# Kernel optimization log

Hardware: AMD Instinct MI355X
Metric: run time of the kernel (lower is better)

## Reference

```python
import jax, jax.numpy as jnp
import numpy as np

B, S = 8, 2048
CLIP, H, BN, NC = 512, 512, 256, 10
LN_EPS = 1e-5


def _ln(x, g, b):
    mu = x.mean(-1, keepdims=True)
    var = ((x - mu) ** 2).mean(-1, keepdims=True)
    return (x - mu) * jax.lax.rsqrt(var + LN_EPS) * g + b


def setup_inputs() -> dict:
    key = jax.random.key(0)
    ks = jax.random.split(key, 16)
    sc = lambda i, shp: jax.random.normal(ks[i], shp, jnp.float32) * 0.02
    inp = {
        "local_feat": jax.random.normal(ks[0], (B, S, CLIP), jnp.float32),
        "coords": jax.random.uniform(ks[1], (B, S, 3), jnp.float32),
        "mask": jax.random.randint(ks[2], (B, S), 0, 2) > 0,
        # node encoder
        "w_enc": sc(3, (CLIP, H)), "b_enc": jnp.zeros((H,), jnp.float32),
        "ln1_g": jnp.ones((H,), jnp.float32), "ln1_b": jnp.zeros((H,), jnp.float32),
        # attention projections
        "wq": sc(4, (H, H)), "bq": jnp.zeros((H,), jnp.float32),
        "wk": sc(5, (H, H)), "bk": jnp.zeros((H,), jnp.float32),
        "wv": sc(6, (H, H)), "bv": jnp.zeros((H,), jnp.float32),
        # bottleneck
        "w_bn": sc(7, (H, BN)), "b_bn": jnp.zeros((BN,), jnp.float32),
        "ln2_g": jnp.ones((BN,), jnp.float32), "ln2_b": jnp.zeros((BN,), jnp.float32),
        # classifier
        "w_c1": sc(8, (BN, BN // 2)), "b_c1": jnp.zeros((BN // 2,), jnp.float32),
        "w_c2": sc(9, (BN // 2, NC)), "b_c2": jnp.zeros((NC,), jnp.float32),
    }
    return inp


def reference(local_feat, coords, mask, w_enc, b_enc, ln1_g, ln1_b,
              wq, bq, wk, bk, wv, bv, w_bn, b_bn, ln2_g, ln2_b,
              w_c1, b_c1, w_c2, b_c2):
    # node encoder (dropout is identity in eval)
    h = jax.nn.relu(_ln(local_feat @ w_enc + b_enc, ln1_g, ln1_b))  # [B,S,H]

    # pairwise euclidean distance on (x,y), exp-modulated adjacency
    pos = coords[:, :, :2]
    diff = pos[:, :, None, :] - pos[:, None, :, :]              # [B,S,S,2]
    sq = jnp.sum(diff * diff, axis=-1)                          # [B,S,S]
    dist = jnp.sqrt(jnp.where(sq > 0, sq, 1.0))
    dist = jnp.where(sq > 0, dist, 0.0)
    spatial_adj = jnp.exp(-dist * 5.0)

    q = h @ wq + bq
    k = h @ wk + bk
    v = h @ wv + bv
    scores = jnp.einsum("bsd,btd->bst", q, k) / jnp.sqrt(jnp.float32(H))
    attn = jax.nn.softmax(scores, axis=-1) * spatial_adj        # [B,S,S]
    attn = jnp.where(mask[:, None, :], 0.0, attn)               # zero padded keys

    h_graph = jnp.einsum("bst,btd->bsd", attn, v)               # [B,S,H]
    out = jax.nn.relu(_ln(h_graph @ w_bn + b_bn, ln2_g, ln2_b)) # [B,S,BN]

    valid = (~mask)[:, :, None].astype(out.dtype)               # [B,S,1]
    pooled = (out * valid).sum(1) / jnp.clip(valid.sum(1), 1e-9, None)

    logits = jax.nn.relu(pooled @ w_c1 + b_c1) @ w_c2 + b_c2    # [B,NC]
    return logits, pooled
```

## Files before the change

kernel.cpp:

```cpp
#include <hip/hip_runtime.h>
#include <hip/hip_bf16.h>
#include <stdint.h>


typedef __hip_bfloat16 bf16_t;
typedef unsigned char u8;
typedef __attribute__((ext_vector_type(8))) short bf16x8;
typedef __attribute__((ext_vector_type(4))) float f32x4;

__device__ __forceinline__ void cp16_to_lds(const void* g, void* lds) {
  __builtin_amdgcn_global_load_lds(
      (__attribute__((address_space(1))) void*)(g),
      (__attribute__((address_space(3))) void*)(lds), 16, 0, 0);
}

__device__ __forceinline__ uint pk2(float a, float b) {
  bf16_t x = __float2bfloat16(a), y = __float2bfloat16(b);
  return ((uint)(*(ushort*)&y) << 16) | (*(ushort*)&x);
}
__device__ __forceinline__ float bflo(uint u) { return __uint_as_float(u << 16); }
__device__ __forceinline__ float bfhi(uint u) { return __uint_as_float(u & 0xffff0000u); }

__global__ __launch_bounds__(256) void gemm_bt(
    const bf16_t* __restrict__ A, const bf16_t* __restrict__ B,
    void* __restrict__ Cv, const float* __restrict__ bias, int biasStride,
    float scale, int K, long sA, long sB, long sC, int ldC, int mode)
{
  __shared__ __align__(16) char smem[32768];
  bf16_t* lA = (bf16_t*)smem;
  bf16_t* lB = (bf16_t*)(smem + 16384);
  const int z = blockIdx.z;
  A += (long)z * sA;
  B += (long)z * sB;
  const float* bz = bias ? bias + (long)z * biasStride : nullptr;
  const int m0 = blockIdx.y * 128, n0 = blockIdx.x * 128;
  const int tid = threadIdx.x;
  const int w = tid >> 6, lane = tid & 63;
  const int wm = w >> 1, wn = w & 1;

  const int rr = tid >> 2;
  const int cc = (((tid & 3) ^ ((tid >> 3) & 3)) * 8);
  const bf16_t* a0 = A + (long)(m0 + rr) * K + cc;
  const bf16_t* b0 = B + (long)(n0 + rr) * K + cc;
  const long rowskip = (long)64 * K;

  char* lAc = (char*)lA;
  char* lBc = (char*)lB;
  const int ofs0 = w * 1024;
  const int ofs1 = 4096 + w * 1024;

  f32x4 acc[4][4] = {};
  const int nkt = K >> 6;
  const int quad = lane >> 4;
  const int rsel = lane & 15;
  const int swz = (rsel >> 1) & 3;
  const int kchunkA = (quad ^ swz) * 8;

  for (int kt = 0; kt < nkt; ++kt) {
    __syncthreads();
    cp16_to_lds(a0,                 lAc + ofs0);
    cp16_to_lds(a0 + rowskip,       lAc + ofs1);
    cp16_to_lds(a0 + 32,            lAc + 8192 + ofs0);
    cp16_to_lds(a0 + 32 + rowskip,  lAc + 8192 + ofs1);
    cp16_to_lds(b0,                 lBc + ofs0);
    cp16_to_lds(b0 + rowskip,       lBc + ofs1);
    cp16_to_lds(b0 + 32,            lBc + 8192 + ofs0);
    cp16_to_lds(b0 + 32 + rowskip,  lBc + 8192 + ofs1);
    a0 += 64; b0 += 64;
    __syncthreads();

#pragma unroll
    for (int p = 0; p < 2; ++p) {
      const int pb = p * 4096;
      bf16x8 af[4], bfr[4];
#pragma unroll
      for (int i = 0; i < 4; ++i) {
        af[i]  = *(const bf16x8*)&lA[pb + (wm * 64 + i * 16 + rsel) * 32 + kchunkA];
        bfr[i] = *(const bf16x8*)&lB[pb + (wn * 64 + i * 16 + rsel) * 32 + kchunkA];
      }
#pragma unroll
      for (int i = 0; i < 4; ++i)
#pragma unroll
        for (int j = 0; j < 4; ++j)
          acc[i][j] = __builtin_amdgcn_mfma_f32_16x16x32_bf16(af[i], bfr[j], acc[i][j], 0, 0, 0);
    }
  }

  const int col = lane & 15;
  float bv4[4];
#pragma unroll
  for (int j = 0; j < 4; ++j) {
    const int ng = n0 + wn * 64 + j * 16 + col;
    bv4[j] = bz ? bz[ng] : 0.0f;
  }

  if (mode == 0) {
    char* stb = smem + w * 2176;
    const int nc0 = n0 + wn * 64;
#pragma unroll
    for (int i = 0; i < 4; ++i) {
      __syncthreads();
      bf16_t* st = (bf16_t*)stb;
#pragma unroll
      for (int j = 0; j < 4; ++j)
#pragma unroll
        for (int r = 0; r < 4; ++r)
          st[(quad * 4 + r) * 68 + j * 16 + col] =
              __float2bfloat16(acc[i][j][r] * scale + bv4[j]);
      __syncthreads();
      const int row16 = lane >> 2, cseg = lane & 3;
      const long mrow = m0 + wm * 64 + i * 16 + row16;
      bf16_t* cp = (bf16_t*)Cv + (long)z * sC + mrow * ldC + nc0 + cseg * 16;
      const char* sp = stb + row16 * 136 + cseg * 32;
#pragma unroll
      for (int hh = 0; hh < 2; ++hh) {
        uint2 aa = *(const uint2*)(sp + hh * 16);
        uint2 bb = *(const uint2*)(sp + hh * 16 + 8);
        uint4 vv; vv.x = aa.x; vv.y = aa.y; vv.z = bb.x; vv.w = bb.y;
        *(uint4*)(cp + hh * 8) = vv;
      }
    }
  } else {
#pragma unroll
    for (int j = 0; j < 4; ++j) {
      const int ng = n0 + wn * 64 + j * 16 + col;
#pragma unroll
      for (int i = 0; i < 4; ++i) {
        const int mg = m0 + wm * 64 + i * 16 + quad * 4;
#pragma unroll
        for (int r = 0; r < 4; ++r)
          ((float*)Cv)[(long)z * sC + (long)(mg + r) * ldC + ng] =
              acc[i][j][r] * scale + bv4[j];
      }
    }
  }
}

__global__ __launch_bounds__(256) void gemm_qkv(
    const bf16_t* __restrict__ A, const bf16_t* __restrict__ wT,
    const float* __restrict__ bias_cat, u8* __restrict__ o8,
    bf16_t* __restrict__ vT)
{
  __shared__ __align__(16) char smem[32768];
  bf16_t* lA = (bf16_t*)smem;
  bf16_t* lB = (bf16_t*)(smem + 16384);
  const int z = blockIdx.z;
  const bf16_t* B = wT + (long)(z + 1) * 262144;
  const float* bz = bias_cat + (long)z * 512;
  const int K = 512;
  const int m0 = blockIdx.y * 128, n0 = blockIdx.x * 128;
  const int tid = threadIdx.x;
  const int w = tid >> 6, lane = tid & 63;
  const int wm = w >> 1, wn = w & 1;

  const int rr = tid >> 2;
  const int cc = (((tid & 3) ^ ((tid >> 3) & 3)) * 8);
  const bf16_t* a0 = A + (long)(m0 + rr) * K + cc;
  const bf16_t* b0 = B + (long)(n0 + rr) * K + cc;
  const long rowskip = (long)64 * K;

  char* lAc = (char*)lA;
  char* lBc = (char*)lB;
  const int ofs0 = w * 1024;
  const int ofs1 = 4096 + w * 1024;

  f32x4 acc[4][4] = {};
  const int quad = lane >> 4;
  const int rsel = lane & 15;
  const int swz = (rsel >> 1) & 3;
  const int kchunkA = (quad ^ swz) * 8;

  for (int kt = 0; kt < 8; ++kt) {
    __syncthreads();
    cp16_to_lds(a0,                 lAc + ofs0);
    cp16_to_lds(a0 + rowskip,       lAc + ofs1);
    cp16_to_lds(a0 + 32,            lAc + 8192 + ofs0);
    cp16_to_lds(a0 + 32 + rowskip,  lAc + 8192 + ofs1);
    cp16_to_lds(b0,                 lBc + ofs0);
    cp16_to_lds(b0 + rowskip,       lBc + ofs1);
    cp16_to_lds(b0 + 32,            lBc + 8192 + ofs0);
    cp16_to_lds(b0 + 32 + rowskip,  lBc + 8192 + ofs1);
    a0 += 64; b0 += 64;
    __syncthreads();

#pragma unroll
    for (int p = 0; p < 2; ++p) {
      const int pb = p * 4096;
      bf16x8 af[4], bfr[4];
#pragma unroll
      for (int i = 0; i < 4; ++i) {
        af[i]  = *(const bf16x8*)&lA[pb + (wm * 64 + i * 16 + rsel) * 32 + kchunkA];
        bfr[i] = *(const bf16x8*)&lB[pb + (wn * 64 + i * 16 + rsel) * 32 + kchunkA];
      }
#pragma unroll
      for (int i = 0; i < 4; ++i)
#pragma unroll
        for (int j = 0; j < 4; ++j)
          acc[i][j] = __builtin_amdgcn_mfma_f32_16x16x32_bf16(af[i], bfr[j], acc[i][j], 0, 0, 0);
    }
  }

  const int col = lane & 15;
  float bv4[4];
#pragma unroll
  for (int j = 0; j < 4; ++j) bv4[j] = bz[n0 + wn * 64 + j * 16 + col];
  const int nc0 = n0 + wn * 64;

  if (z < 2) {
    u8* stb = (u8*)(smem + w * 2176);
    u8* O = o8 + (long)z * 8388608;
#pragma unroll
    for (int i = 0; i < 4; ++i) {
      __syncthreads();
#pragma unroll
      for (int j = 0; j < 4; ++j) {
        uint pk = 0;
        pk = __builtin_amdgcn_cvt_pk_fp8_f32(acc[i][j][0] + bv4[j],
                                             acc[i][j][1] + bv4[j], pk, false);
        pk = __builtin_amdgcn_cvt_pk_fp8_f32(acc[i][j][2] + bv4[j],
                                             acc[i][j][3] + bv4[j], pk, true);
        stb[(quad * 4 + 0) * 72 + j * 16 + col] = (u8)(pk);
        stb[(quad * 4 + 1) * 72 + j * 16 + col] = (u8)(pk >> 8);
        stb[(quad * 4 + 2) * 72 + j * 16 + col] = (u8)(pk >> 16);
        stb[(quad * 4 + 3) * 72 + j * 16 + col] = (u8)(pk >> 24);
      }
      __syncthreads();
      const int trow = lane >> 2, seg = lane & 3;
      const long mrow = m0 + wm * 64 + i * 16 + trow;
      *(uint4*)(O + mrow * 512 + nc0 + seg * 16) =
          *(const uint4*)(stb + trow * 72 + seg * 16);
    }
  } else {
    bf16_t* st = (bf16_t*)(smem + w * 2176);
    const int bt = blockIdx.y >> 4;
    const int t0g = (m0 & 2047) + wm * 64;
#pragma unroll
    for (int j = 0; j < 4; ++j) {
      __syncthreads();
#pragma unroll
      for (int i = 0; i < 4; ++i) {
        uint2 v2;
        v2.x = pk2(acc[i][j][0] + bv4[j], acc[i][j][1] + bv4[j]);
        v2.y = pk2(acc[i][j][2] + bv4[j], acc[i][j][3] + bv4[j]);
        *(uint2*)&st[col * 68 + i * 16 + quad * 4] = v2;
      }
      __syncthreads();
      const int drow = lane >> 2, seg = lane & 3;
      const int d = nc0 + j * 16 + drow;
      bf16_t* dst = vT + ((long)(bt * 512 + d)) * 2048 + t0g;
#pragma unroll
      for (int rd = 0; rd < 2; ++rd)
        *(uint4*)(dst + rd * 32 + seg * 8) =
            *(const uint4*)((const char*)st + drow * 136 + rd * 64 + seg * 16);
    }
  }
}

__global__ __launch_bounds__(256) void gemm_sc_fp8(
    const u8* __restrict__ A, const u8* __restrict__ B,
    bf16_t* __restrict__ C, float scale)
{
  __shared__ __align__(16) char smem[32768];
  const int K = 512;
  const int z = blockIdx.z;
  A += (long)z * 1048576;
  B += (long)z * 1048576;
  const int m0 = blockIdx.y * 128, n0 = blockIdx.x * 128;
  const int tid = threadIdx.x;
  const int w = tid >> 6, lane = tid & 63;
  const int wm = w >> 1, wn = w & 1;

  const int rr = tid >> 2;
  const int ccB = (((tid & 3) ^ ((tid >> 3) & 3)) * 16);
  const u8* a0 = A + (long)(m0 + rr) * K + ccB;
  const u8* b0 = B + (long)(n0 + rr) * K + ccB;
  const long rowskip = (long)64 * K;

  char* lAc = smem;
  char* lBc = smem + 16384;
  const int ofs0 = w * 1024;
  const int ofs1 = 4096 + w * 1024;

  f32x4 acc[4][4] = {};
  const int quad = lane >> 4;
  const int rsel = lane & 15;
  const int swz = (rsel >> 1) & 3;

  for (int kt = 0; kt < 4; ++kt) {
    __syncthreads();
    cp16_to_lds(a0,                  lAc + ofs0);
    cp16_to_lds(a0 + rowskip,        lAc + ofs1);
    cp16_to_lds(a0 + 64,             lAc + 8192 + ofs0);
    cp16_to_lds(a0 + 64 + rowskip,   lAc + 8192 + ofs1);
    cp16_to_lds(b0,                  lBc + ofs0);
    cp16_to_lds(b0 + rowskip,        lBc + ofs1);
    cp16_to_lds(b0 + 64,             lBc + 8192 + ofs0);
    cp16_to_lds(b0 + 64 + rowskip,   lBc + 8192 + ofs1);
    a0 += 128; b0 += 128;
    __syncthreads();

#pragma unroll
    for (int p = 0; p < 2; ++p) {
      const int pb = p * 8192;
#pragma unroll
      for (int ks = 0; ks < 2; ++ks) {
        const int gr = ((ks * 2 + (quad >> 1)) ^ swz) * 16 + (quad & 1) * 8;
        long av[4], bv[4];
#pragma unroll
        for (int i = 0; i < 4; ++i) {
          av[i] = *(const long*)(lAc + pb + (wm * 64 + i * 16 + rsel) * 64 + gr);
          bv[i] = *(const long*)(lBc + pb + (wn * 64 + i * 16 + rsel) * 64 + gr);
        }
#pragma unroll
        for (int i = 0; i < 4; ++i)
#pragma unroll
          for (int j = 0; j < 4; ++j)
            acc[i][j] = __builtin_amdgcn_mfma_f32_16x16x32_fp8_fp8(av[i], bv[j], acc[i][j], 0, 0, 0);
      }
    }
  }

  const int col = lane & 15;
  char* stb = smem + w * 2176;
  const int nc0 = n0 + wn * 64;
#pragma unroll
  for (int i = 0; i < 4; ++i) {
    __syncthreads();
    bf16_t* st = (bf16_t*)stb;
#pragma unroll
    for (int j = 0; j < 4; ++j)
#pragma unroll
      for (int r = 0; r < 4; ++r)
        st[(quad * 4 + r) * 68 + j * 16 + col] =
            __float2bfloat16(acc[i][j][r] * scale);
    __syncthreads();
    const int row16 = lane >> 2, cseg = lane & 3;
    const long mrow = m0 + wm * 64 + i * 16 + row16;
    bf16_t* cp = C + (long)z * 4194304 + mrow * 2048 + nc0 + cseg * 16;
    const char* sp = stb + row16 * 136 + cseg * 32;
#pragma unroll
    for (int hh = 0; hh < 2; ++hh) {
      uint2 aa = *(const uint2*)(sp + hh * 16);
      uint2 bb = *(const uint2*)(sp + hh * 16 + 8);
      uint4 vv; vv.x = aa.x; vv.y = aa.y; vv.z = bb.x; vv.w = bb.y;
      *(uint4*)(cp + hh * 8) = vv;
    }
  }
}

__global__ __launch_bounds__(256) void weight_prep(
    const float* __restrict__ w0, const float* __restrict__ w1,
    const float* __restrict__ w2, const float* __restrict__ w3,
    const float* __restrict__ w4,
    const float* __restrict__ bq, const float* __restrict__ bk,
    const float* __restrict__ bv,
    bf16_t* __restrict__ outT, float* __restrict__ bias_cat)
{
  const int z = blockIdx.z;
  const int N = (z == 4) ? 256 : 512;
  if (z == 4 && blockIdx.y >= 4) return;
  const float* in = (z == 0) ? w0 : (z == 1) ? w1 : (z == 2) ? w2 : (z == 3) ? w3 : w4;
  bf16_t* out = outT + (long)z * 262144;
  const int k0 = blockIdx.x * 64, n0 = blockIdx.y * 64;
  __shared__ bf16_t tile[64 * 66];
  const int tid = threadIdx.x;
  const int r = tid >> 2, c4 = tid & 3;
  const float* src = in + (long)(k0 + r) * N + n0 + c4 * 16;
  uint* dst = (uint*)&tile[r * 66 + c4 * 16];
  float4 f0 = ((const float4*)src)[0], f1 = ((const float4*)src)[1];
  float4 f2 = ((const float4*)src)[2], f3 = ((const float4*)src)[3];
  dst[0] = pk2(f0.x, f0.y); dst[1] = pk2(f0.z, f0.w);
  dst[2] = pk2(f1.x, f1.y); dst[3] = pk2(f1.z, f1.w);
  dst[4] = pk2(f2.x, f2.y); dst[5] = pk2(f2.z, f2.w);
  dst[6] = pk2(f3.x, f3.y); dst[7] = pk2(f3.z, f3.w);
  __syncthreads();
  bf16_t* og = out + (long)(n0 + r) * 512 + k0 + c4 * 16;
  uint ov[8];
#pragma unroll
  for (int j = 0; j < 16; j += 2) {
    const ushort lo = *(const ushort*)&tile[(c4 * 16 + j) * 66 + r];
    const ushort hi = *(const ushort*)&tile[(c4 * 16 + j + 1) * 66 + r];
    ov[j >> 1] = ((uint)hi << 16) | lo;
  }
  uint4 o0, o1;
  o0.x = ov[0]; o0.y = ov[1]; o0.z = ov[2]; o0.w = ov[3];
  o1.x = ov[4]; o1.y = ov[5]; o1.z = ov[6]; o1.w = ov[7];
  ((uint4*)og)[0] = o0;
  ((uint4*)og)[1] = o1;
  if (z >= 1 && z <= 3 && blockIdx.x == 0 && blockIdx.y == 0) {
    const float* bs = (z == 1) ? bq : (z == 2) ? bk : bv;
    bias_cat[(z - 1) * 512 + tid] = bs[tid];
    bias_cat[(z - 1) * 512 + 256 + tid] = bs[256 + tid];
  }
}

__global__ __launch_bounds__(256) void cast_bf16_v(
    const float4* __restrict__ in, uint2* __restrict__ o, int n4) {
  const int i = blockIdx.x * 256 + threadIdx.x;
  if (i < n4) {
    const float4 f = in[i];
    uint2 r; r.x = pk2(f.x, f.y); r.y = pk2(f.z, f.w);
    o[i] = r;
  }
}

__global__ __launch_bounds__(256) void ln_relu_h(
    bf16_t* __restrict__ X, const float* __restrict__ g, const float* __restrict__ b)
{
  const int tid = threadIdx.x;
  const int lane = tid & 63, w = tid >> 6;
  const long row = (long)blockIdx.x * 4 + w;
  bf16_t* xp = X + row * 512 + lane * 8;
  const uint4 pkv = *(const uint4*)xp;
  const uint va[4] = {pkv.x, pkv.y, pkv.z, pkv.w};
  float v[8];
  float s = 0.0f, q = 0.0f;
#pragma unroll
  for (int i = 0; i < 4; ++i) {
    v[2 * i] = bflo(va[i]); v[2 * i + 1] = bfhi(va[i]);
    s += v[2 * i] + v[2 * i + 1];
    q += v[2 * i] * v[2 * i] + v[2 * i + 1] * v[2 * i + 1];
  }
  for (int o = 32; o; o >>= 1) { s += __shfl_down(s, o); q += __shfl_down(q, o); }
  s = __shfl(s, 0); q = __shfl(q, 0);
  const float mu = s * (1.0f / 512.0f);
  const float rs = rsqrtf(q * (1.0f / 512.0f) - mu * mu + 1e-5f);
  const float4 g0 = ((const float4*)(g + lane * 8))[0], g1 = ((const float4*)(g + lane * 8))[1];
  const float4 b0 = ((const float4*)(b + lane * 8))[0], b1 = ((const float4*)(b + lane * 8))[1];
  const float gg[8] = {g0.x, g0.y, g0.z, g0.w, g1.x, g1.y, g1.z, g1.w};
  const float bb[8] = {b0.x, b0.y, b0.z, b0.w, b1.x, b1.y, b1.z, b1.w};
  uint ov[4];
#pragma unroll
  for (int i = 0; i < 4; ++i) {
    const float y0 = fmaxf((v[2 * i] - mu) * rs * gg[2 * i] + bb[2 * i], 0.0f);
    const float y1 = fmaxf((v[2 * i + 1] - mu) * rs * gg[2 * i + 1] + bb[2 * i + 1], 0.0f);
    ov[i] = pk2(y0, y1);
  }
  uint4 st; st.x = ov[0]; st.y = ov[1]; st.z = ov[2]; st.w = ov[3];
  *(uint4*)xp = st;
}

__global__ __launch_bounds__(256) void softmax_adj(
    bf16_t* __restrict__ SC, const float* __restrict__ coords,
    const int* __restrict__ mask)
{
  const int bs = blockIdx.x;
  const int b = bs >> 11, s = bs & 2047;
  const long base = (long)bs * 2048;
  const int tid = threadIdx.x;
  const uint4 pkv = *(const uint4*)(SC + base + tid * 8);
  const uint va[4] = {pkv.x, pkv.y, pkv.z, pkv.w};
  float rv[8];
  float mx = -3.0e38f;
#pragma unroll
  for (int i = 0; i < 4; ++i) {
    rv[2 * i] = bflo(va[i]); rv[2 * i + 1] = bfhi(va[i]);
    mx = fmaxf(mx, fmaxf(rv[2 * i], rv[2 * i + 1]));
  }
  for (int o = 32; o; o >>= 1) mx = fmaxf(mx, __shfl_down(mx, o));
  __shared__ float sm[8];
  const int w = tid >> 6, lane = tid & 63;
  if (!lane) sm[w] = mx;
  __syncthreads();
  mx = fmaxf(fmaxf(sm[0], sm[1]), fmaxf(sm[2], sm[3]));
  float sum = 0.0f;
#pragma unroll
  for (int i = 0; i < 8; ++i) { rv[i] = __expf(rv[i] - mx); sum += rv[i]; }
  for (int o = 32; o; o >>= 1) sum += __shfl_down(sum, o);
  if (!lane) sm[4 + w] = sum;
  __syncthreads();
  const float inv = 1.0f / (sm[4] + sm[5] + sm[6] + sm[7]);
  const float px = coords[((long)b * 2048 + s) * 3];
  const float py = coords[((long)b * 2048 + s) * 3 + 1];
  const int t0 = tid * 8;
  const float* cb = coords + ((long)b * 2048 + t0) * 3;
  const int* mb = mask + b * 2048 + t0;
  uint ov[4];
#pragma unroll
  for (int i = 0; i < 8; ++i) {
    const float dx = px - cb[i * 3], dy = py - cb[i * 3 + 1];
    const float adj = __expf(-5.0f * sqrtf(dx * dx + dy * dy));
    const float val = mb[i] ? 0.0f : rv[i] * inv * adj;
    bf16_t bt = __float2bfloat16(val);
    const ushort u = *(const ushort*)&bt;
    if (i & 1) ov[i >> 1] |= ((uint)u << 16);
    else       ov[i >> 1] = u;
  }
  uint4 st; st.x = ov[0]; st.y = ov[1]; st.z = ov[2]; st.w = ov[3];
  *(uint4*)(SC + base + t0) = st;
}

__global__ __launch_bounds__(256) void ln2_pool(
    const float* __restrict__ X, const float* __restrict__ g, const float* __restrict__ bt,
    const int* __restrict__ mask, float* __restrict__ pacc)
{
  const int tid = threadIdx.x;
  const int row0 = blockIdx.x * 16;
  const int w = tid >> 6, lane = tid & 63;
  __shared__ float sm[8];
  const float gv = g[tid], bv = bt[tid];
  float acc = 0.0f;
  for (int r = 0; r < 16; ++r) {
    const int row = row0 + r;
    const float x = X[(long)row * 256 + tid];
    float s = x, q = x * x;
    for (int o = 32; o; o >>= 1) { s += __shfl_down(s, o); q += __shfl_down(q, o); }
    if (!lane) { sm[w] = s; sm[4 + w] = q; }
    __syncthreads();
    const float S = sm[0] + sm[1] + sm[2] + sm[3];
    const float Q = sm[4] + sm[5] + sm[6] + sm[7];
    const float mu = S * (1.0f / 256.0f);
    const float rs = rsqrtf(Q * (1.0f / 256.0f) - mu * mu + 1e-5f);
    const float y = fmaxf((x - mu) * rs * gv + bv, 0.0f);
    if (!mask[row]) acc += y;
    __syncthreads();
  }
  atomicAdd(&pacc[(row0 >> 11) * 256 + tid], acc);
}

__global__ __launch_bounds__(256) void classifier_k(
    const float* __restrict__ pacc, const int* __restrict__ mask,
    const float* __restrict__ w1, const float* __restrict__ b1,
    const float* __restrict__ w2, const float* __restrict__ b2,
    float* __restrict__ out)
{
  const int tid = threadIdx.x;
  __shared__ float pooled[2048];
  __shared__ float hidden[1024];
  __shared__ float cnt[8];
  if (tid < 8) cnt[tid] = 0.0f;
  __syncthreads();
  {
    const int* mb = mask + tid * 64;
    int c = 0;
#pragma unroll 8
    for (int i = 0; i < 64; ++i) c += mb[i] ? 0 : 1;
    atomicAdd(&cnt[tid >> 5], (float)c);
  }
  __syncthreads();
  for (int i = tid; i < 2048; i += 256) {
    const float p = pacc[i] / fmaxf(cnt[i >> 8], 1e-9f);
    pooled[i] = p;
    out[80 + i] = p;
  }
  __syncthreads();
  for (int o = tid; o < 1024; o += 256) {
    const int bb = o >> 7, j = o & 127;
    float s = b1[j];
    const float* pb = pooled + bb * 256;
    for (int c = 0; c < 256; ++c) s += pb[c] * w1[c * 128 + j];
    hidden[o] = fmaxf(s, 0.0f);
  }
  __syncthreads();
  if (tid < 80) {
    const int bb = tid / 10, j = tid - bb * 10;
    float s = b2[j];
    const float* hb = hidden + bb * 128;
    for (int c = 0; c < 128; ++c) s += hb[c] * w2[c * 10 + j];
    out[tid] = s;
  }
}

extern "C" void kernel_launch(void* const* d_in, const int* in_sizes, int n_in,
                              void* d_out, int out_size, void* d_ws, size_t ws_size,
                              hipStream_t stream)
{
  const float* lf   = (const float*)d_in[0];
  const float* co   = (const float*)d_in[1];
  const int*   mk   = (const int*)d_in[2];
  const float* wenc = (const float*)d_in[3];
  const float* benc = (const float*)d_in[4];
  const float* g1   = (const float*)d_in[5];
  const float* be1  = (const float*)d_in[6];
  const float* wq   = (const float*)d_in[7];
  const float* bq   = (const float*)d_in[8];
  const float* wk   = (const float*)d_in[9];
  const float* bk   = (const float*)d_in[10];
  const float* wv   = (const float*)d_in[11];
  const float* bvp  = (const float*)d_in[12];
  const float* wbn  = (const float*)d_in[13];
  const float* bbn  = (const float*)d_in[14];
  const float* g2   = (const float*)d_in[15];
  const float* be2  = (const float*)d_in[16];
  const float* w1   = (const float*)d_in[17];
  const float* b1   = (const float*)d_in[18];
  const float* w2   = (const float*)d_in[19];
  const float* b2   = (const float*)d_in[20];
  float* out = (float*)d_out;
  char* ws = (char*)d_ws;

  bf16_t* featb = (bf16_t*)(ws + 0);
  bf16_t* wT    = (bf16_t*)(ws + 16777216);
  bf16_t* wencT = wT;
  bf16_t* wbnT  = wT + 4 * 262144;
  float*  bias_cat = (float*)(ws + 19398656);
  bf16_t* h     = (bf16_t*)(ws + 19404800);
  u8*     q8    = (u8*)(ws + 36182016);
  bf16_t* vT    = (bf16_t*)(ws + 52959232);
  bf16_t* sc    = (bf16_t*)(ws + 69736448);
  bf16_t* hg    = (bf16_t*)(ws + 0);
  float*  bnp   = (float*)(ws + 36182016);
  float*  pacc  = (float*)(ws + 52959232);

  if (ws_size < 136845312) return;

  cast_bf16_v<<<8192, 256, 0, stream>>>((const float4*)lf, (uint2*)featb, 2097152);
  weight_prep<<<dim3(8, 8, 5), 256, 0, stream>>>(wenc, wq, wk, wv, wbn, bq, bk, bvp,
                                                 wT, bias_cat);

  gemm_bt<<<dim3(4, 128, 1), 256, 0, stream>>>(featb, wencT, h, benc, 0, 1.0f, 512,
                                               0, 0, 0, 512, 0);
  ln_relu_h<<<4096, 256, 0, stream>>>(h, g1, be1);
  gemm_qkv<<<dim3(4, 128, 3), 256, 0, stream>>>(h, wT, bias_cat, q8, vT);
  gemm_sc_fp8<<<dim3(16, 16, 8), 256, 0, stream>>>(q8, q8 + 8388608, sc,
                                                   0.044194173824159216f);
  softmax_adj<<<16384, 256, 0, stream>>>(sc, co, mk);
  gemm_bt<<<dim3(4, 16, 8), 256, 0, stream>>>(sc, vT, hg, nullptr, 0, 1.0f, 2048,
                                              4194304, 1048576, 1048576, 512, 0);
  gemm_bt<<<dim3(2, 128, 1), 256, 0, stream>>>(hg, wbnT, bnp, bbn, 0, 1.0f, 512,
                                               0, 0, 0, 256, 2);
  hipMemsetAsync(pacc, 0, 8192, stream);
  ln2_pool<<<1024, 256, 0, stream>>>(bnp, g2, be2, mk, pacc);
  classifier_k<<<1, 256, 0, stream>>>(pacc, mk, w1, b1, w2, b2, out);
}
```

Baseline: 365.3 us.

## Use FP8 for attention probabilities and V in the attn@V GEMM

V is now written from the QKV GEMM as transposed FP8 instead of bf16, and the softmax kernel emits FP8 attention weights pre-scaled by 256 into a separate buffer. The attn@V product reuses a generalized FP8 GEMM kernel, with an unscale factor of 1/256, in place of the bf16 GEMM. This halves the bytes read by the largest GEMM and uses the faster FP8 matrix instructions, at the cost of lower precision in the attention weights and values.

```diff
diff --git a/kernel.cpp b/kernel.cpp
--- a/kernel.cpp
+++ b/kernel.cpp
@@ -139,7 +139,7 @@
 __global__ __launch_bounds__(256) void gemm_qkv(
     const bf16_t* __restrict__ A, const bf16_t* __restrict__ wT,
     const float* __restrict__ bias_cat, u8* __restrict__ o8,
-    bf16_t* __restrict__ vT)
+    u8* __restrict__ vT8)
 {
   __shared__ __align__(16) char smem[32768];
   bf16_t* lA = (bf16_t*)smem;
@@ -231,7 +231,7 @@
           *(const uint4*)(stb + trow * 72 + seg * 16);
     }
   } else {
-    bf16_t* st = (bf16_t*)(smem + w * 2176);
+    u8* st8 = (u8*)(smem + w * 2176);
     const int bt = blockIdx.y >> 4;
     const int t0g = (m0 & 2047) + wm * 64;
 #pragma unroll
@@ -239,32 +239,31 @@
       __syncthreads();
 #pragma unroll
       for (int i = 0; i < 4; ++i) {
-        uint2 v2;
-        v2.x = pk2(acc[i][j][0] + bv4[j], acc[i][j][1] + bv4[j]);
-        v2.y = pk2(acc[i][j][2] + bv4[j], acc[i][j][3] + bv4[j]);
-        *(uint2*)&st[col * 68 + i * 16 + quad * 4] = v2;
+        uint pk = 0;
+        pk = __builtin_amdgcn_cvt_pk_fp8_f32(acc[i][j][0] + bv4[j],
+                                             acc[i][j][1] + bv4[j], pk, false);
+        pk = __builtin_amdgcn_cvt_pk_fp8_f32(acc[i][j][2] + bv4[j],
+                                             acc[i][j][3] + bv4[j], pk, true);
+        *(uint*)&st8[col * 72 + i * 16 + quad * 4] = pk;
       }
       __syncthreads();
       const int drow = lane >> 2, seg = lane & 3;
       const int d = nc0 + j * 16 + drow;
-      bf16_t* dst = vT + ((long)(bt * 512 + d)) * 2048 + t0g;
-#pragma unroll
-      for (int rd = 0; rd < 2; ++rd)
-        *(uint4*)(dst + rd * 32 + seg * 8) =
-            *(const uint4*)((const char*)st + drow * 136 + rd * 64 + seg * 16);
-    }
-  }
-}
-
-__global__ __launch_bounds__(256) void gemm_sc_fp8(
+      u8* dst = vT8 + ((long)(bt * 512 + d)) * 2048 + t0g;
+      *(uint4*)(dst + seg * 16) = *(const uint4*)(st8 + drow * 72 + seg * 16);
+    }
+  }
+}
+
+__global__ __launch_bounds__(256) void gemm_fp8(
     const u8* __restrict__ A, const u8* __restrict__ B,
-    bf16_t* __restrict__ C, float scale)
+    bf16_t* __restrict__ C, float scale, int K,
+    long sA, long sB, long sC, int ldC)
 {
   __shared__ __align__(16) char smem[32768];
-  const int K = 512;
   const int z = blockIdx.z;
-  A += (long)z * 1048576;
-  B += (long)z * 1048576;
+  A += (long)z * sA;
+  B += (long)z * sB;
   const int m0 = blockIdx.y * 128, n0 = blockIdx.x * 128;
   const int tid = threadIdx.x;
   const int w = tid >> 6, lane = tid & 63;
@@ -286,7 +285,8 @@
   const int rsel = lane & 15;
   const int swz = (rsel >> 1) & 3;
 
-  for (int kt = 0; kt < 4; ++kt) {
+  const int nkt = K >> 7;
+  for (int kt = 0; kt < nkt; ++kt) {
     __syncthreads();
     cp16_to_lds(a0,                  lAc + ofs0);
     cp16_to_lds(a0 + rowskip,        lAc + ofs1);
@@ -336,7 +336,7 @@
     __syncthreads();
     const int row16 = lane >> 2, cseg = lane & 3;
     const long mrow = m0 + wm * 64 + i * 16 + row16;
-    bf16_t* cp = C + (long)z * 4194304 + mrow * 2048 + nc0 + cseg * 16;
+    bf16_t* cp = C + (long)z * sC + mrow * ldC + nc0 + cseg * 16;
     const char* sp = stb + row16 * 136 + cseg * 32;
 #pragma unroll
     for (int hh = 0; hh < 2; ++hh) {
@@ -441,8 +441,8 @@
 }
 
 __global__ __launch_bounds__(256) void softmax_adj(
-    bf16_t* __restrict__ SC, const float* __restrict__ coords,
-    const int* __restrict__ mask)
+    const bf16_t* __restrict__ SC, u8* __restrict__ A8,
+    const float* __restrict__ coords, const int* __restrict__ mask)
 {
   const int bs = blockIdx.x;
   const int b = bs >> 11, s = bs & 2047;
@@ -469,25 +469,27 @@
   for (int o = 32; o; o >>= 1) sum += __shfl_down(sum, o);
   if (!lane) sm[4 + w] = sum;
   __syncthreads();
-  const float inv = 1.0f / (sm[4] + sm[5] + sm[6] + sm[7]);
+  const float inv = 256.0f / (sm[4] + sm[5] + sm[6] + sm[7]);
   const float px = coords[((long)b * 2048 + s) * 3];
   const float py = coords[((long)b * 2048 + s) * 3 + 1];
   const int t0 = tid * 8;
   const float* cb = coords + ((long)b * 2048 + t0) * 3;
   const int* mb = mask + b * 2048 + t0;
-  uint ov[4];
+  float ov[8];
 #pragma unroll
   for (int i = 0; i < 8; ++i) {
     const float dx = px - cb[i * 3], dy = py - cb[i * 3 + 1];
     const float adj = __expf(-5.0f * sqrtf(dx * dx + dy * dy));
-    const float val = mb[i] ? 0.0f : rv[i] * inv * adj;
-    bf16_t bt = __float2bfloat16(val);
-    const ushort u = *(const ushort*)&bt;
-    if (i & 1) ov[i >> 1] |= ((uint)u << 16);
-    else       ov[i >> 1] = u;
-  }
-  uint4 st; st.x = ov[0]; st.y = ov[1]; st.z = ov[2]; st.w = ov[3];
-  *(uint4*)(SC + base + t0) = st;
+    ov[i] = mb[i] ? 0.0f : rv[i] * inv * adj;
+  }
+  uint2 st;
+  uint p0 = 0, p1 = 0;
+  p0 = __builtin_amdgcn_cvt_pk_fp8_f32(ov[0], ov[1], p0, false);
+  p0 = __builtin_amdgcn_cvt_pk_fp8_f32(ov[2], ov[3], p0, true);
+  p1 = __builtin_amdgcn_cvt_pk_fp8_f32(ov[4], ov[5], p1, false);
+  p1 = __builtin_amdgcn_cvt_pk_fp8_f32(ov[6], ov[7], p1, true);
+  st.x = p0; st.y = p1;
+  *(uint2*)(A8 + base + t0) = st;
 }
 
 __global__ __launch_bounds__(256) void ln2_pool(
@@ -594,15 +596,16 @@
   bf16_t* wencT = wT;
   bf16_t* wbnT  = wT + 4 * 262144;
   float*  bias_cat = (float*)(ws + 19398656);
-  bf16_t* h     = (bf16_t*)(ws + 19404800);
-  u8*     q8    = (u8*)(ws + 36182016);
-  bf16_t* vT    = (bf16_t*)(ws + 52959232);
-  bf16_t* sc    = (bf16_t*)(ws + 69736448);
+  bf16_t* h     = (bf16_t*)(ws + 19406848);
+  u8*     q8    = (u8*)(ws + 36184064);
+  u8*     vT8   = (u8*)(ws + 52961280);
+  bf16_t* sc    = (bf16_t*)(ws + 61349888);
+  u8*     at8   = (u8*)(ws + 128458752);
   bf16_t* hg    = (bf16_t*)(ws + 0);
-  float*  bnp   = (float*)(ws + 36182016);
-  float*  pacc  = (float*)(ws + 52959232);
-
-  if (ws_size < 136845312) return;
+  float*  bnp   = (float*)(ws + 36184064);
+  float*  pacc  = (float*)(ws + 52961280);
+
+  if (ws_size < 162013184) return;
 
   cast_bf16_v<<<8192, 256, 0, stream>>>((const float4*)lf, (uint2*)featb, 2097152);
   weight_prep<<<dim3(8, 8, 5), 256, 0, stream>>>(wenc, wq, wk, wv, wbn, bq, bk, bvp,
@@ -611,12 +614,13 @@
   gemm_bt<<<dim3(4, 128, 1), 256, 0, stream>>>(featb, wencT, h, benc, 0, 1.0f, 512,
                                                0, 0, 0, 512, 0);
   ln_relu_h<<<4096, 256, 0, stream>>>(h, g1, be1);
-  gemm_qkv<<<dim3(4, 128, 3), 256, 0, stream>>>(h, wT, bias_cat, q8, vT);
-  gemm_sc_fp8<<<dim3(16, 16, 8), 256, 0, stream>>>(q8, q8 + 8388608, sc,
-                                                   0.044194173824159216f);
-  softmax_adj<<<16384, 256, 0, stream>>>(sc, co, mk);
-  gemm_bt<<<dim3(4, 16, 8), 256, 0, stream>>>(sc, vT, hg, nullptr, 0, 1.0f, 2048,
-                                              4194304, 1048576, 1048576, 512, 0);
+  gemm_qkv<<<dim3(4, 128, 3), 256, 0, stream>>>(h, wT, bias_cat, q8, vT8);
+  gemm_fp8<<<dim3(16, 16, 8), 256, 0, stream>>>(q8, q8 + 8388608, sc,
+                                                0.044194173824159216f, 512,
+                                                1048576, 1048576, 4194304, 2048);
+  softmax_adj<<<16384, 256, 0, stream>>>(sc, at8, co, mk);
+  gemm_fp8<<<dim3(4, 16, 8), 256, 0, stream>>>(at8, vT8, hg, 0.00390625f, 2048,
+                                               4194304, 1048576, 1048576, 512);
   gemm_bt<<<dim3(2, 128, 1), 256, 0, stream>>>(hg, wbnT, bnp, bbn, 0, 1.0f, 512,
                                                0, 0, 0, 256, 2);
   hipMemsetAsync(pacc, 0, 8192, stream);
```

After: 364.6 us. No clear change (-0.2%).
